# Kernel optimization log

Measured on AMD Instinct MI355X. Metric: run time of the kernel, lower is better.

## Reference

```python
import jax, jax.numpy as jnp
import numpy as np

NHEADS = 4
WS = 5  # kernel_size


def setup_inputs() -> dict:
    key = jax.random.key(0)
    ks = jax.random.split(key, 7)
    T, C, H, W, S = 4, 256, 256, 256, 9
    x = jax.random.normal(ks[0], (T, C, H, W), dtype=jnp.float32)
    sims = jax.random.uniform(ks[1], (T, S, H, W), dtype=jnp.float32)
    flows = jnp.zeros((T, 1, 2, H, W), dtype=jnp.int32)  # wt = shape[-4]//2 = 0
    w_std = 1.0 / np.sqrt(C)
    Wq = jax.random.normal(ks[2], (C, C), dtype=jnp.float32) * w_std
    Wk = jax.random.normal(ks[3], (C, C), dtype=jnp.float32) * w_std
    Wv = jax.random.normal(ks[4], (C, C), dtype=jnp.float32) * w_std
    Wp = jax.random.normal(ks[5], (C, C), dtype=jnp.float32) * w_std
    return {"x": x, "sims": sims, "flows": flows, "Wq": Wq, "Wk": Wk, "Wv": Wv, "Wp": Wp}


def reference(x, sims, flows, Wq, Wk, Wv, Wp):
    # x: [T,C,H,W], sims: [T,S,H,W], flows: [T,1,2,H,W] (zeros -> wt=0)
    T, C, H, W = x.shape
    hd = C // NHEADS
    r = WS // 2
    scale = hd ** -0.5
    xp = jnp.transpose(x, (0, 2, 3, 1))                 # [T,H,W,C]
    q = (xp @ Wq).reshape(T, H, W, NHEADS, hd) * scale  # [T,H,W,nh,hd]
    k = (xp @ Wk).reshape(T, H, W, NHEADS, hd)
    v = (xp @ Wv).reshape(T, H, W, NHEADS, hd)
    simsp = jnp.transpose(sims, (0, 2, 3, 1))           # [T,H,W,S]
    ih = jnp.arange(H)
    iw = jnp.arange(W)
    offsets = [(di, dj) for di in range(-r, r + 1) for dj in range(-r, r + 1)]

    attn_cols, sim_cols = [], []
    for di, dj in offsets:  # fixed 25-offset window (not a data loop)
        ii = jnp.clip(ih + di, 0, H - 1)
        jj = jnp.clip(iw + dj, 0, W - 1)
        ksh = k[:, ii][:, :, jj]                        # [T,H,W,nh,hd]
        attn_cols.append(jnp.einsum('thwnc,thwnc->thwn', q, ksh))
        ssh = simsp[:, ii][:, :, jj]                    # [T,H,W,S]
        sim_cols.append(jnp.einsum('thws,thws->thw', simsp, ssh))
    attn = jnp.stack(attn_cols, axis=-1)                # [T,H,W,nh,K]
    sim_attn = jnp.stack(sim_cols, axis=-1)[..., None, :]  # [T,H,W,1,K]

    # attn_rw_stnls: exp-shift, reweight by superpixel similarity, renormalize
    attn = jnp.exp(attn - jnp.max(attn, axis=-1, keepdims=True))
    attn = attn * sim_attn
    attn = attn / (1e-10 + jnp.sum(attn, axis=-1, keepdims=True))

    out = jnp.zeros((T, H, W, NHEADS, hd), dtype=x.dtype)
    for kk, (di, dj) in enumerate(offsets):
        ii = jnp.clip(ih + di, 0, H - 1)
        jj = jnp.clip(iw + dj, 0, W - 1)
        vsh = v[:, ii][:, :, jj]                        # [T,H,W,nh,hd]
        out = out + attn[..., kk:kk + 1] * vsh
    out = out.reshape(T, H, W, C) @ Wp                  # output projection
    return jnp.transpose(out, (0, 3, 1, 2))             # [T,C,H,W]
```

## Files before the change

kernel.cpp:

```cpp
#include <hip/hip_runtime.h>

#define T_  4
#define C_  256
#define H_  256
#define W_  256
#define S_  9
#define HW_ (H_*W_)
#define NH  4
#define HD  64
#define KK  25

typedef unsigned short ushort_t;
typedef __bf16 bf16x8 __attribute__((ext_vector_type(8)));
typedef float  f32x4  __attribute__((ext_vector_type(4)));

__device__ __forceinline__ unsigned short f2bf(float f) {
    unsigned u = __builtin_bit_cast(unsigned, f);
    u += 0x7fffu + ((u >> 16) & 1u);
    return (unsigned short)(u >> 16);
}
__device__ __forceinline__ float bflo(unsigned u) {
    return __builtin_bit_cast(float, u << 16);
}
__device__ __forceinline__ float bfhi(unsigned u) {
    return __builtin_bit_cast(float, u & 0xffff0000u);
}
__device__ __forceinline__ void gload16(const ushort_t* g, ushort_t* l) {
    __builtin_amdgcn_global_load_lds(
        (const __attribute__((address_space(1))) void*)g,
        (__attribute__((address_space(3))) void*)l, 16, 0, 0);
}

__global__ __launch_bounds__(256)
void prep_w(const float* __restrict__ Wq, const float* __restrict__ Wk,
            const float* __restrict__ Wv, const float* __restrict__ Wp,
            ushort_t* __restrict__ Wt)
{
    int r = blockIdx.x;
    int m = r >> 8, co = r & 255;
    int ci = threadIdx.x;
    const float* W = (m == 0) ? Wq : ((m == 1) ? Wk : ((m == 2) ? Wv : Wp));
    float s = (m == 0) ? 0.125f : 1.0f;
    Wt[(size_t)r * 256 + ci] = f2bf(W[(size_t)ci * 256 + co] * s);
}

__global__ __launch_bounds__(256)
void cast_x(const float* __restrict__ X, ushort_t* __restrict__ Xt)
{
    int hw0 = blockIdx.x * 64, c0 = blockIdx.y * 64, t = blockIdx.z;
    __shared__ ushort_t lds[64][68];
    int tid = threadIdx.x;
    const float* xb = X + ((size_t)t * C_ + c0) * HW_ + hw0;
#pragma unroll
    for (int i = 0; i < 4; i++) {
        int idx = tid + i * 256;
        int c = idx >> 4, col4 = idx & 15;
        float4 v = *(const float4*)(xb + (size_t)c * HW_ + col4 * 4);
        ushort4 u = make_ushort4(f2bf(v.x), f2bf(v.y), f2bf(v.z), f2bf(v.w));
        *(ushort4*)&lds[c][col4 * 4] = u;
    }
    __syncthreads();
    ushort_t* ob = Xt + ((size_t)t * HW_ + hw0) * C_ + c0;
#pragma unroll
    for (int i = 0; i < 4; i++) {
        int idx = tid + i * 256;
        int hw = idx >> 4, c4 = idx & 15;
        ushort4 u = make_ushort4(lds[c4 * 4 + 0][hw], lds[c4 * 4 + 1][hw],
                                 lds[c4 * 4 + 2][hw], lds[c4 * 4 + 3][hw]);
        *(ushort4*)(ob + (size_t)hw * C_ + c4 * 4) = u;
    }
}

__global__ __launch_bounds__(256)
void gemm_mfma(const ushort_t* __restrict__ A, const ushort_t* __restrict__ Bt,
               ushort_t* __restrict__ o0, ushort_t* __restrict__ o1,
               ushort_t* __restrict__ o2, float* __restrict__ of, int mode)
{
    __shared__ ushort_t As[128 * 32];
    __shared__ ushort_t Bs[128 * 32];
    const int tid = threadIdx.x, ln = tid & 63, wv = tid >> 6;
    const int n0  = blockIdx.x * 128;
    const int co0 = blockIdx.y * 128;
    const int m_off = (wv & 1) * 64, n_off = (wv >> 1) * 64;

    f32x4 acc[4][4];
#pragma unroll
    for (int i = 0; i < 4; i++)
#pragma unroll
        for (int j = 0; j < 4; j++) acc[i][j] = (f32x4){0.f, 0.f, 0.f, 0.f};

    const int srow = ln >> 2, scol = (ln & 3) * 8;
    const ushort_t* gA = A  + (size_t)(n0  + srow) * 256 + scol;
    const ushort_t* gB = Bt + (size_t)(co0 + srow) * 256 + scol;
    const int quad = ln >> 4, lm = ln & 15;

#pragma unroll
    for (int k0 = 0; k0 < 256; k0 += 32) {
#pragma unroll
        for (int c = 0; c < 2; c++) {
            int rr = wv * 32 + c * 16;
            gload16(gA + (size_t)rr * 256 + k0, As + rr * 32);
            gload16(gB + (size_t)rr * 256 + k0, Bs + rr * 32);
        }
        __syncthreads();
        bf16x8 af[4], bfr[4];
#pragma unroll
        for (int mt = 0; mt < 4; mt++)
            af[mt] = *(const bf16x8*)&As[(m_off + mt * 16 + lm) * 32 + quad * 8];
#pragma unroll
        for (int nt = 0; nt < 4; nt++)
            bfr[nt] = *(const bf16x8*)&Bs[(n_off + nt * 16 + lm) * 32 + quad * 8];
#pragma unroll
        for (int mt = 0; mt < 4; mt++)
#pragma unroll
            for (int nt = 0; nt < 4; nt++)
                acc[mt][nt] = __builtin_amdgcn_mfma_f32_16x16x32_bf16(
                    af[mt], bfr[nt], acc[mt][nt], 0, 0, 0);
        __syncthreads();
    }

    if (mode == 0) {
        int arr = co0 >> 8;
        ushort_t* op = (arr == 0) ? o0 : ((arr == 1) ? o1 : o2);
        int cobase = (co0 & 255) + n_off;
#pragma unroll
        for (int mt = 0; mt < 4; mt++) {
            int nb = n0 + m_off + mt * 16 + quad * 4;
#pragma unroll
            for (int nt = 0; nt < 4; nt++) {
                int ci = cobase + nt * 16 + lm;
#pragma unroll
                for (int r = 0; r < 4; r++)
                    op[(size_t)(nb + r) * 256 + ci] = f2bf(acc[mt][nt][r]);
            }
        }
    } else {
#pragma unroll
        for (int mt = 0; mt < 4; mt++) {
            int nb = n0 + m_off + mt * 16 + quad * 4;
            int tt = nb >> 16, hwb = nb & (HW_ - 1);
            float* ob = of + (size_t)tt * (C_ * (size_t)HW_) + hwb;
#pragma unroll
            for (int nt = 0; nt < 4; nt++) {
                int cg = co0 + n_off + nt * 16 + lm;
                float4 val = make_float4(acc[mt][nt][0], acc[mt][nt][1],
                                         acc[mt][nt][2], acc[mt][nt][3]);
                *(float4*)(ob + (size_t)cg * HW_) = val;
            }
        }
    }
}

__global__ __launch_bounds__(256)
void attn2(const ushort_t* __restrict__ q, const ushort_t* __restrict__ k,
           const ushort_t* __restrict__ v, const float* __restrict__ sims,
           ushort_t* __restrict__ ao)
{
    const int w0 = blockIdx.x * 64, h = blockIdx.y, t = blockIdx.z;
    const int tid = threadIdx.x, ln = tid & 63, head = tid >> 6;
    const int w = w0 + ln, hw = h * W_ + w;
    const size_t npix = (size_t)t * HW_ + hw;

    __shared__ float lw[NH][KK][64];
    __shared__ float sw[KK][64];

    {
        const float* sp = sims + (size_t)t * S_ * HW_;
        float s0[S_];
#pragma unroll
        for (int s = 0; s < S_; s++) s0[s] = sp[s * HW_ + hw];
#pragma unroll 1
        for (int e = head; e < KK; e += NH) {
            int di = e / 5 - 2, dj = e % 5 - 2;
            int h2 = min(max(h + di, 0), H_ - 1);
            int w2 = min(max(w + dj, 0), W_ - 1);
            int o = h2 * W_ + w2;
            float a = 0.f;
#pragma unroll
            for (int s = 0; s < S_; s++) a += s0[s] * sp[s * HW_ + o];
            sw[e][ln] = a;
        }
    }

    const ushort_t* qb = q + npix * 256 + head * HD;
    float qf[HD];
#pragma unroll
    for (int i = 0; i < 8; i++) {
        uint4 x = *(const uint4*)(qb + i * 8);
        qf[i*8+0] = bflo(x.x); qf[i*8+1] = bfhi(x.x);
        qf[i*8+2] = bflo(x.y); qf[i*8+3] = bfhi(x.y);
        qf[i*8+4] = bflo(x.z); qf[i*8+5] = bfhi(x.z);
        qf[i*8+6] = bflo(x.w); qf[i*8+7] = bfhi(x.w);
    }

    const size_t tbase = (size_t)t * HW_ * 256;
    const ushort_t* kb = k + tbase + head * HD;

#pragma unroll 1
    for (int e = 0; e < KK; e++) {
        int di = e / 5 - 2, dj = e % 5 - 2;
        int h2 = min(max(h + di, 0), H_ - 1);
        int w2 = min(max(w + dj, 0), W_ - 1);
        int o = h2 * W_ + w2;
        const ushort_t* kp = kb + (size_t)o * 256;
        float a = 0.f;
#pragma unroll
        for (int i = 0; i < 8; i++) {
            uint4 kv = *(const uint4*)(kp + i * 8);
            a += qf[i*8+0] * bflo(kv.x); a += qf[i*8+1] * bfhi(kv.x);
            a += qf[i*8+2] * bflo(kv.y); a += qf[i*8+3] * bfhi(kv.y);
            a += qf[i*8+4] * bflo(kv.z); a += qf[i*8+5] * bfhi(kv.z);
            a += qf[i*8+6] * bflo(kv.w); a += qf[i*8+7] * bfhi(kv.w);
        }
        lw[head][e][ln] = a;
    }
    __syncthreads();

    float mx = -1e30f;
#pragma unroll 1
    for (int e = 0; e < KK; e++) mx = fmaxf(mx, lw[head][e][ln]);
    float sum = 0.f;
#pragma unroll 1
    for (int e = 0; e < KK; e++) {
        float p = __expf(lw[head][e][ln] - mx) * sw[e][ln];
        sum += p;
        lw[head][e][ln] = p;
    }
    const float inv = 1.0f / (1e-10f + sum);

    const ushort_t* vb = v + tbase + head * HD;
    ushort_t* ab = ao + npix * 256 + head * HD;
#pragma unroll 1
    for (int half = 0; half < 2; half++) {
        float oa[32];
#pragma unroll
        for (int i = 0; i < 32; i++) oa[i] = 0.f;
#pragma unroll 1
        for (int e = 0; e < KK; e++) {
            int di = e / 5 - 2, dj = e % 5 - 2;
            int h2 = min(max(h + di, 0), H_ - 1);
            int w2 = min(max(w + dj, 0), W_ - 1);
            int o = h2 * W_ + w2;
            float wgt = lw[head][e][ln] * inv;
            const ushort_t* vp = vb + (size_t)o * 256 + half * 32;
#pragma unroll
            for (int i = 0; i < 4; i++) {
                uint4 vv = *(const uint4*)(vp + i * 8);
                oa[i*8+0] += wgt * bflo(vv.x); oa[i*8+1] += wgt * bfhi(vv.x);
                oa[i*8+2] += wgt * bflo(vv.y); oa[i*8+3] += wgt * bfhi(vv.y);
                oa[i*8+4] += wgt * bflo(vv.z); oa[i*8+5] += wgt * bfhi(vv.z);
                oa[i*8+6] += wgt * bflo(vv.w); oa[i*8+7] += wgt * bfhi(vv.w);
            }
        }
        unsigned pk[16];
#pragma unroll
        for (int j = 0; j < 16; j++)
            pk[j] = (unsigned)f2bf(oa[2*j]) | ((unsigned)f2bf(oa[2*j+1]) << 16);
        uint4* stp = (uint4*)(ab + half * 32);
#pragma unroll
        for (int i = 0; i < 4; i++)
            stp[i] = make_uint4(pk[i*4+0], pk[i*4+1], pk[i*4+2], pk[i*4+3]);
    }
}

extern "C" void kernel_launch(void* const* d_in, const int* in_sizes, int n_in,
                              void* d_out, int out_size, void* d_ws, size_t ws_size,
                              hipStream_t stream)
{
    const float* x    = (const float*)d_in[0];
    const float* sims = (const float*)d_in[1];
    const float* Wq   = (const float*)d_in[3];
    const float* Wk   = (const float*)d_in[4];
    const float* Wv   = (const float*)d_in[5];
    const float* Wp   = (const float*)d_in[6];
    float* out = (float*)d_out;

    const size_t NPIX = (size_t)T_ * HW_;
    const size_t NCH  = NPIX * 256;

    ushort_t* Wt = (ushort_t*)d_ws;
    ushort_t* Xt = (ushort_t*)((char*)d_ws + (1 << 20));
    ushort_t* qq = Xt + NCH;
    ushort_t* kk = qq + NCH;
    ushort_t* vv = kk + NCH;
    ushort_t* ao = vv + NCH;

    prep_w<<<1024, 256, 0, stream>>>(Wq, Wk, Wv, Wp, Wt);
    cast_x<<<dim3(HW_ / 64, C_ / 64, T_), 256, 0, stream>>>(x, Xt);

    gemm_mfma<<<dim3(NPIX / 128, 6), 256, 0, stream>>>(Xt, Wt, qq, kk, vv, nullptr, 0);

    attn2<<<dim3(W_ / 64, H_, T_), 256, 0, stream>>>(qq, kk, vv, sims, ao);

    gemm_mfma<<<dim3(NPIX / 128, 2), 256, 0, stream>>>(ao, Wt + 768 * 256,
                                                       nullptr, nullptr, nullptr, out, 1);
}
```

Measured before the change: 1.549 ms.

## Store q/k/v channel-major so attention lanes read coalesced neighbor pixels

The QKV GEMM now writes q, k and v planar ([channel][pixel]) instead of pixel-major, packing four consecutive pixels per ushort4 store. The attention kernel is rewritten so each lane walks the head channels and reads one bf16 per neighbor offset. Adjacent lanes then touch adjacent pixels, which makes the loads coalesced across the wavefront, and logits stay in registers rather than LDS. The cost is many 2-byte scalar loads instead of 16-byte vector loads, higher register pressure from 25 logits and offsets, and the output normalization moved to the end.

```diff
diff --git a/kernel.cpp b/kernel.cpp
--- a/kernel.cpp
+++ b/kernel.cpp
@@ -9,6 +9,7 @@
 #define NH  4
 #define HD  64
 #define KK  25
+#define NPIX_ (T_*HW_)
 
 typedef unsigned short ushort_t;
 typedef __bf16 bf16x8 __attribute__((ext_vector_type(8)));
@@ -24,6 +25,9 @@
 }
 __device__ __forceinline__ float bfhi(unsigned u) {
     return __builtin_bit_cast(float, u & 0xffff0000u);
+}
+__device__ __forceinline__ float bfs(ushort_t u) {
+    return __builtin_bit_cast(float, ((unsigned)u) << 16);
 }
 __device__ __forceinline__ void gload16(const ushort_t* g, ushort_t* l) {
     __builtin_amdgcn_global_load_lds(
@@ -120,18 +124,17 @@
     }
 
     if (mode == 0) {
-        int arr = co0 >> 8;
-        ushort_t* op = (arr == 0) ? o0 : ((arr == 1) ? o1 : o2);
-        int cobase = (co0 & 255) + n_off;
 #pragma unroll
         for (int mt = 0; mt < 4; mt++) {
             int nb = n0 + m_off + mt * 16 + quad * 4;
 #pragma unroll
             for (int nt = 0; nt < 4; nt++) {
-                int ci = cobase + nt * 16 + lm;
-#pragma unroll
-                for (int r = 0; r < 4; r++)
-                    op[(size_t)(nb + r) * 256 + ci] = f2bf(acc[mt][nt][r]);
+                int co = co0 + n_off + nt * 16 + lm;
+                int arr = co >> 8, ci = co & 255;
+                ushort_t* op = (arr == 0) ? o0 : ((arr == 1) ? o1 : o2);
+                ushort4 u = make_ushort4(f2bf(acc[mt][nt][0]), f2bf(acc[mt][nt][1]),
+                                         f2bf(acc[mt][nt][2]), f2bf(acc[mt][nt][3]));
+                *(ushort4*)(op + (size_t)ci * NPIX_ + nb) = u;
             }
         }
     } else {
@@ -152,16 +155,15 @@
 }
 
 __global__ __launch_bounds__(256)
-void attn2(const ushort_t* __restrict__ q, const ushort_t* __restrict__ k,
+void attn3(const ushort_t* __restrict__ q, const ushort_t* __restrict__ k,
            const ushort_t* __restrict__ v, const float* __restrict__ sims,
            ushort_t* __restrict__ ao)
 {
     const int w0 = blockIdx.x * 64, h = blockIdx.y, t = blockIdx.z;
-    const int tid = threadIdx.x, ln = tid & 63, head = tid >> 6;
+    const int tid = threadIdx.x, ln = tid & 63;
+    const int head = __builtin_amdgcn_readfirstlane(tid >> 6);
     const int w = w0 + ln, hw = h * W_ + w;
-    const size_t npix = (size_t)t * HW_ + hw;
-
-    __shared__ float lw[NH][KK][64];
+
     __shared__ float sw[KK][64];
 
     {
@@ -182,84 +184,71 @@
         }
     }
 
-    const ushort_t* qb = q + npix * 256 + head * HD;
-    float qf[HD];
-#pragma unroll
-    for (int i = 0; i < 8; i++) {
-        uint4 x = *(const uint4*)(qb + i * 8);
-        qf[i*8+0] = bflo(x.x); qf[i*8+1] = bfhi(x.x);
-        qf[i*8+2] = bflo(x.y); qf[i*8+3] = bfhi(x.y);
-        qf[i*8+4] = bflo(x.z); qf[i*8+5] = bfhi(x.z);
-        qf[i*8+6] = bflo(x.w); qf[i*8+7] = bfhi(x.w);
-    }
-
-    const size_t tbase = (size_t)t * HW_ * 256;
-    const ushort_t* kb = k + tbase + head * HD;
-
-#pragma unroll 1
+    int pb[KK];
+#pragma unroll
     for (int e = 0; e < KK; e++) {
-        int di = e / 5 - 2, dj = e % 5 - 2;
+        const int di = e / 5 - 2, dj = e % 5 - 2;
         int h2 = min(max(h + di, 0), H_ - 1);
         int w2 = min(max(w + dj, 0), W_ - 1);
-        int o = h2 * W_ + w2;
-        const ushort_t* kp = kb + (size_t)o * 256;
-        float a = 0.f;
-#pragma unroll
-        for (int i = 0; i < 8; i++) {
-            uint4 kv = *(const uint4*)(kp + i * 8);
-            a += qf[i*8+0] * bflo(kv.x); a += qf[i*8+1] * bfhi(kv.x);
-            a += qf[i*8+2] * bflo(kv.y); a += qf[i*8+3] * bfhi(kv.y);
-            a += qf[i*8+4] * bflo(kv.z); a += qf[i*8+5] * bfhi(kv.z);
-            a += qf[i*8+6] * bflo(kv.w); a += qf[i*8+7] * bfhi(kv.w);
-        }
-        lw[head][e][ln] = a;
-    }
+        pb[e] = (h2 * W_ + w2) * 2;
+    }
+
+    const size_t cstride = (size_t)NPIX_ * 2;
+    const char* kt = (const char*)k + (size_t)(head * HD) * cstride + (size_t)t * HW_ * 2;
+    const char* qt = (const char*)q + (size_t)(head * HD) * cstride
+                                    + ((size_t)t * HW_ + hw) * 2;
+
+    float lg[KK];
+#pragma unroll
+    for (int e = 0; e < KK; e++) lg[e] = 0.f;
+
+#pragma unroll 4
+    for (int c = 0; c < HD; c++) {
+        float qf = bfs(*(const ushort_t*)(qt + (size_t)c * cstride));
+        const char* kc = kt + (size_t)c * cstride;
+#pragma unroll
+        for (int e = 0; e < KK; e++)
+            lg[e] += qf * bfs(*(const ushort_t*)(kc + pb[e]));
+    }
+
     __syncthreads();
 
-    float mx = -1e30f;
+    float mx = lg[0];
+#pragma unroll
+    for (int e = 1; e < KK; e++) mx = fmaxf(mx, lg[e]);
+    float sum = 0.f;
+#pragma unroll
+    for (int e = 0; e < KK; e++) {
+        float p = __expf(lg[e] - mx) * sw[e][ln];
+        sum += p;
+        lg[e] = p;
+    }
+    const float inv = 1.0f / (1e-10f + sum);
+
+    const char* vt = (const char*)v + (size_t)(head * HD) * cstride + (size_t)t * HW_ * 2;
+    ushort_t* ab = ao + ((size_t)t * HW_ + hw) * 256 + head * HD;
+
 #pragma unroll 1
-    for (int e = 0; e < KK; e++) mx = fmaxf(mx, lw[head][e][ln]);
-    float sum = 0.f;
-#pragma unroll 1
-    for (int e = 0; e < KK; e++) {
-        float p = __expf(lw[head][e][ln] - mx) * sw[e][ln];
-        sum += p;
-        lw[head][e][ln] = p;
-    }
-    const float inv = 1.0f / (1e-10f + sum);
-
-    const ushort_t* vb = v + tbase + head * HD;
-    ushort_t* ab = ao + npix * 256 + head * HD;
-#pragma unroll 1
-    for (int half = 0; half < 2; half++) {
-        float oa[32];
-#pragma unroll
-        for (int i = 0; i < 32; i++) oa[i] = 0.f;
-#pragma unroll 1
+    for (int cc = 0; cc < 4; cc++) {
+        const char* vc = vt + (size_t)(cc * 16) * cstride;
+        float oa[16];
+#pragma unroll
+        for (int i = 0; i < 16; i++) oa[i] = 0.f;
+#pragma unroll
         for (int e = 0; e < KK; e++) {
-            int di = e / 5 - 2, dj = e % 5 - 2;
-            int h2 = min(max(h + di, 0), H_ - 1);
-            int w2 = min(max(w + dj, 0), W_ - 1);
-            int o = h2 * W_ + w2;
-            float wgt = lw[head][e][ln] * inv;
-            const ushort_t* vp = vb + (size_t)o * 256 + half * 32;
-#pragma unroll
-            for (int i = 0; i < 4; i++) {
-                uint4 vv = *(const uint4*)(vp + i * 8);
-                oa[i*8+0] += wgt * bflo(vv.x); oa[i*8+1] += wgt * bfhi(vv.x);
-                oa[i*8+2] += wgt * bflo(vv.y); oa[i*8+3] += wgt * bfhi(vv.y);
-                oa[i*8+4] += wgt * bflo(vv.z); oa[i*8+5] += wgt * bfhi(vv.z);
-                oa[i*8+6] += wgt * bflo(vv.w); oa[i*8+7] += wgt * bfhi(vv.w);
-            }
-        }
-        unsigned pk[16];
-#pragma unroll
-        for (int j = 0; j < 16; j++)
-            pk[j] = (unsigned)f2bf(oa[2*j]) | ((unsigned)f2bf(oa[2*j+1]) << 16);
-        uint4* stp = (uint4*)(ab + half * 32);
-#pragma unroll
-        for (int i = 0; i < 4; i++)
-            stp[i] = make_uint4(pk[i*4+0], pk[i*4+1], pk[i*4+2], pk[i*4+3]);
+            float wgt = lg[e];
+#pragma unroll
+            for (int i = 0; i < 16; i++)
+                oa[i] += wgt * bfs(*(const ushort_t*)(vc + (size_t)i * cstride + pb[e]));
+        }
+        unsigned pk[8];
+#pragma unroll
+        for (int j = 0; j < 8; j++)
+            pk[j] = (unsigned)f2bf(oa[2 * j] * inv)
+                  | ((unsigned)f2bf(oa[2 * j + 1] * inv) << 16);
+        uint4* stp = (uint4*)(ab + cc * 16);
+        stp[0] = make_uint4(pk[0], pk[1], pk[2], pk[3]);
+        stp[1] = make_uint4(pk[4], pk[5], pk[6], pk[7]);
     }
 }
 
@@ -275,8 +264,7 @@
     const float* Wp   = (const float*)d_in[6];
     float* out = (float*)d_out;
 
-    const size_t NPIX = (size_t)T_ * HW_;
-    const size_t NCH  = NPIX * 256;
+    const size_t NCH = (size_t)NPIX_ * 256;
 
     ushort_t* Wt = (ushort_t*)d_ws;
     ushort_t* Xt = (ushort_t*)((char*)d_ws + (1 << 20));
@@ -288,10 +276,10 @@
     prep_w<<<1024, 256, 0, stream>>>(Wq, Wk, Wv, Wp, Wt);
     cast_x<<<dim3(HW_ / 64, C_ / 64, T_), 256, 0, stream>>>(x, Xt);
 
-    gemm_mfma<<<dim3(NPIX / 128, 6), 256, 0, stream>>>(Xt, Wt, qq, kk, vv, nullptr, 0);
-
-    attn2<<<dim3(W_ / 64, H_, T_), 256, 0, stream>>>(qq, kk, vv, sims, ao);
-
-    gemm_mfma<<<dim3(NPIX / 128, 2), 256, 0, stream>>>(ao, Wt + 768 * 256,
-                                                       nullptr, nullptr, nullptr, out, 1);
-}
+    gemm_mfma<<<dim3(NPIX_ / 128, 6), 256, 0, stream>>>(Xt, Wt, qq, kk, vv, nullptr, 0);
+
+    attn3<<<dim3(W_ / 64, H_, T_), 256, 0, stream>>>(qq, kk, vv, sims, ao);
+
+    gemm_mfma<<<dim3(NPIX_ / 128, 2), 256, 0, stream>>>(ao, Wt + 768 * 256,
+                                                        nullptr, nullptr, nullptr, out, 1);
+}
```

After: 4.208 ms. 2.72x slower.
